# Performance work log

Hardware: AMD Instinct MI355X
Metric: run time of the kernel (lower is better)

The kernel has to match this reference:

```python
import jax, jax.numpy as jnp
import numpy as np

D_MODEL = 512
D_FF = 2048
NUM_EXPERTS = 8
TOP_K = 2


def setup_inputs() -> dict:
    key = jax.random.key(0)
    ks = jax.random.split(key, 6)
    scale = 0.02
    x = jax.random.normal(ks[0], (4, 8192, D_MODEL), dtype=jnp.float32)
    gate_w = jax.random.normal(ks[1], (D_MODEL, NUM_EXPERTS), dtype=jnp.float32) * scale
    w1 = jax.random.normal(ks[2], (NUM_EXPERTS, D_MODEL, D_FF), dtype=jnp.float32) * scale
    b1 = jnp.zeros((NUM_EXPERTS, D_FF), dtype=jnp.float32)
    w2 = jax.random.normal(ks[3], (NUM_EXPERTS, D_FF, D_MODEL), dtype=jnp.float32) * scale
    b2 = jnp.zeros((NUM_EXPERTS, D_MODEL), dtype=jnp.float32)
    return {"x": x, "gate_w": gate_w, "w1": w1, "b1": b1, "w2": w2, "b2": b2}


def reference(x, gate_w, w1, b1, w2, b2):
    B, S, D = x.shape
    xt = x.reshape(-1, D)                                  # [T, D]
    logits = xt @ gate_w                                   # [T, E]
    probs = jax.nn.softmax(logits, axis=-1)
    top_p, top_i = jax.lax.top_k(probs, TOP_K)             # [T, K]
    top_p = top_p / jnp.sum(top_p, axis=-1, keepdims=True)
    # per-token combine weight for each expert: [T, E]
    w_te = jnp.sum(jax.nn.one_hot(top_i, NUM_EXPERTS, dtype=xt.dtype) * top_p[..., None], axis=1)
    out = jnp.zeros_like(xt)
    for e in range(NUM_EXPERTS):  # small fixed loop over experts
        h = jax.nn.gelu(xt @ w1[e] + b1[e], approximate=False)  # [T, d_ff]
        y = h @ w2[e] + b2[e]                                   # [T, D]
        out = out + w_te[:, e:e + 1] * y
    return out.reshape(B, S, D)
```

## Files before the change

kernel.cpp:

```cpp
#include <hip/hip_runtime.h>
#include <math.h>

#define T_TOK 32768
#define DM 512
#define DFF 2048
#define NE 8
#define MAXTILES 528

typedef __attribute__((ext_vector_type(8))) short short8;
typedef __attribute__((ext_vector_type(4))) float f32x4;

__device__ __forceinline__ unsigned int f2bf1(float f) {
  union { float f; unsigned int u; } x; x.f = f;
  return (x.u + 0x7fffu + ((x.u >> 16) & 1u)) >> 16;
}

#define GLOAD(src, dst) \
  __builtin_amdgcn_global_load_lds((const __attribute__((address_space(1))) unsigned int*)(src), \
                                   (__attribute__((address_space(3))) unsigned int*)(dst), 16, 0, 0)
#define WAITVM(N) asm volatile("s_waitcnt vmcnt(" #N ")" ::: "memory")
#define BARRIER() asm volatile("s_barrier" ::: "memory")

__global__ void tcvt_kernel(const float* __restrict__ src, unsigned short* __restrict__ dst,
                            int R, int C) {
  __shared__ float tile[32][33];
  int e = blockIdx.z;
  const float* s = src + (size_t)e * R * C;
  unsigned short* d = dst + (size_t)e * R * C;
  int c0 = blockIdx.x * 32, r0 = blockIdx.y * 32;
  int tx = threadIdx.x, ty = threadIdx.y;
#pragma unroll
  for (int i = 0; i < 4; ++i)
    tile[ty + i * 8][tx] = s[(size_t)(r0 + ty + i * 8) * C + c0 + tx];
  __syncthreads();
#pragma unroll
  for (int i = 0; i < 4; ++i)
    d[(size_t)(c0 + ty + i * 8) * R + r0 + tx] = (unsigned short)f2bf1(tile[tx][ty + i * 8]);
}

__global__ __launch_bounds__(1024) void gate_kernel(
    const float* __restrict__ x, const float* __restrict__ gw,
    int* __restrict__ cnt, int* __restrict__ tok, float* __restrict__ wgt,
    unsigned int* __restrict__ xb) {
  __shared__ int lcnt[NE];
  __shared__ int lbase[NE];
  __shared__ int wslot[16][2];
  __shared__ int winfo[16][2];
  __shared__ float wval[16][2];
  int tid = threadIdx.x;
  int wid = tid >> 6, lane = tid & 63;
  int t = blockIdx.x * 16 + wid;
  if (tid < NE) lcnt[tid] = 0;
  __syncthreads();

  float acc[NE];
#pragma unroll
  for (int e = 0; e < NE; ++e) acc[e] = 0.f;
  const float* xr = x + (size_t)t * DM;
  unsigned int* xbr = xb + (size_t)t * (DM / 2);
#pragma unroll
  for (int j = 0; j < 4; ++j) {
    int d0 = j * 128 + lane * 2;
    float2 xv = *(const float2*)(xr + d0);
    const float* g0 = gw + d0 * NE;
#pragma unroll
    for (int e = 0; e < NE; ++e) acc[e] += xv.x * g0[e] + xv.y * g0[NE + e];
    xbr[j * 64 + lane] = f2bf1(xv.x) | (f2bf1(xv.y) << 16);
  }
#pragma unroll
  for (int off = 32; off >= 1; off >>= 1) {
#pragma unroll
    for (int e = 0; e < NE; ++e) acc[e] += __shfl_xor(acc[e], off);
  }
  if (lane == 0) {
    int e0 = 0; float l0 = acc[0];
#pragma unroll
    for (int e = 1; e < NE; ++e) if (acc[e] > l0) { l0 = acc[e]; e0 = e; }
    int e1 = (e0 == 0) ? 1 : 0; float l1 = acc[e1];
#pragma unroll
    for (int e = 0; e < NE; ++e) if (e != e0 && acc[e] > l1) { l1 = acc[e]; e1 = e; }
    float w0 = 1.f / (1.f + expf(l1 - l0));
    winfo[wid][0] = e0; winfo[wid][1] = e1;
    wval[wid][0] = w0;  wval[wid][1] = 1.f - w0;
    wslot[wid][0] = atomicAdd(&lcnt[e0], 1);
    wslot[wid][1] = atomicAdd(&lcnt[e1], 1);
  }
  __syncthreads();
  if (tid < NE) lbase[tid] = atomicAdd(&cnt[tid * 64], lcnt[tid]);
  __syncthreads();
  if (lane == 0) {
    int e0 = winfo[wid][0], e1 = winfo[wid][1];
    int p0 = lbase[e0] + wslot[wid][0];
    int p1 = lbase[e1] + wslot[wid][1];
    tok[e0 * T_TOK + p0] = t; wgt[e0 * T_TOK + p0] = wval[wid][0];
    tok[e1 * T_TOK + p1] = t; wgt[e1 * T_TOK + p1] = wval[wid][1];
  }
}

__global__ void plan_kernel(const int* __restrict__ cnt, int* __restrict__ tile_base) {
  if (threadIdx.x == 0 && blockIdx.x == 0) {
    int tb = 0;
    for (int e = 0; e < NE; ++e) { tile_base[e] = tb; tb += (cnt[e * 64] + 127) >> 7; }
    tile_base[NE] = tb;
  }
}

__global__ __launch_bounds__(256) void gemm1_kernel(
    const unsigned int* __restrict__ xb, const unsigned short* __restrict__ w1t,
    const float* __restrict__ b1, const int* __restrict__ cnt,
    const int* __restrict__ tok, const int* __restrict__ tile_base,
    unsigned short* __restrict__ H, int tile_lo) {
  int bid = (int)blockIdx.x;
  int nt = bid & 15;
  int gt = tile_lo + (bid >> 4);
  if (gt >= tile_base[NE]) return;
  int e = 0;
#pragma unroll
  for (int k = 0; k < NE - 1; ++k) e += (gt >= tile_base[k + 1]) ? 1 : 0;
  int tloc = gt - tile_base[e];
  int ce = cnt[e * 64];
  int m0 = tloc * 128;
  int n0 = nt * 128;

  __shared__ char Lds[5 * 16384];

  int tid = (int)threadIdx.x;
  int lane = tid & 63;
  int wid = tid >> 6;
  int wm = wid & 1, wn = wid >> 1;
  int fl = lane & 15, q = lane >> 4;
  int sxy = ((q ^ ((fl >> 1) & 3)) << 4);

  const int* tokg = tok + e * T_TOK;
  int r0 = tid >> 2, r1 = 64 + (tid >> 2);
  int sl = tid & 3;
  int ss0 = sl ^ ((r0 >> 1) & 3);
  int ss1 = sl ^ ((r1 >> 1) & 3);
  int t0 = tokg[min(m0 + r0, ce - 1)];
  int t1 = tokg[min(m0 + r1, ce - 1)];
  const char* asrc0 = (const char*)xb + (size_t)t0 * 1024 + ss0 * 16;
  const char* asrc1 = (const char*)xb + (size_t)t1 * 1024 + ss1 * 16;
  const char* bsrc0 = (const char*)w1t + ((size_t)e * DFF + n0 + r0) * 1024 + ss0 * 16;
  const char* bsrc1 = (const char*)w1t + ((size_t)e * DFF + n0 + r1) * 1024 + ss1 * 16;

  int aoff[4], boff[4];
#pragma unroll
  for (int i = 0; i < 4; ++i) {
    aoff[i] = (wm * 64 + i * 16 + fl) * 64 + sxy;
    boff[i] = 8192 + (wn * 64 + i * 16 + fl) * 64 + sxy;
  }

  f32x4 acc[4][4];
#pragma unroll
  for (int a = 0; a < 4; ++a)
#pragma unroll
    for (int b = 0; b < 4; ++b) acc[a][b] = (f32x4){0.f, 0.f, 0.f, 0.f};

#define STAGE1(bi, ti) do { \
    char* base_ = Lds + (bi) * 16384; size_t ko_ = (size_t)(ti) * 64; \
    GLOAD(asrc0 + ko_, base_ + tid * 16);        \
    GLOAD(asrc1 + ko_, base_ + 4096 + tid * 16); \
    GLOAD(bsrc0 + ko_, base_ + 8192 + tid * 16); \
    GLOAD(bsrc1 + ko_, base_ + 12288 + tid * 16); } while (0)

#define COMP1(bi) do { \
    const char* base_ = Lds + (bi) * 16384; \
    short8 a[4], b[4]; \
    _Pragma("unroll") for (int i = 0; i < 4; ++i) { \
      a[i] = *(const short8*)(base_ + aoff[i]); \
      b[i] = *(const short8*)(base_ + boff[i]); } \
    _Pragma("unroll") for (int mf = 0; mf < 4; ++mf) \
    _Pragma("unroll") for (int nf = 0; nf < 4; ++nf) \
      acc[mf][nf] = __builtin_amdgcn_mfma_f32_16x16x32_bf16(a[mf], b[nf], acc[mf][nf], 0, 0, 0); \
  } while (0)

  STAGE1(0, 0); STAGE1(1, 1); STAGE1(2, 2); STAGE1(3, 3);
  int c0 = 0, c1 = 4;
  for (int t = 0; t < 13; ++t) {
    WAITVM(12);
    BARRIER();
    if (t + 4 < 16) { STAGE1(c1, t + 4); c1 = (c1 == 4) ? 0 : c1 + 1; }
    COMP1(c0); c0 = (c0 == 4) ? 0 : c0 + 1;
  }
  WAITVM(8);  BARRIER(); COMP1(c0); c0 = (c0 == 4) ? 0 : c0 + 1;
  WAITVM(4);  BARRIER(); COMP1(c0); c0 = (c0 == 4) ? 0 : c0 + 1;
  WAITVM(0);  BARRIER(); COMP1(c0);
#undef STAGE1
#undef COMP1

  size_t hrow0 = (size_t)(gt - tile_lo) * 128;
#pragma unroll
  for (int nf = 0; nf < 4; ++nf) {
    float bias = b1[e * DFF + n0 + wn * 64 + nf * 16 + fl];
    int col = n0 + wn * 64 + nf * 16 + fl;
#pragma unroll
    for (int mf = 0; mf < 4; ++mf)
#pragma unroll
      for (int j = 0; j < 4; ++j) {
        int row = wm * 64 + mf * 16 + q * 4 + j;
        float v = acc[mf][nf][j] + bias;
        v = 0.5f * v * (1.f + erff(v * 0.70710678118654752f));
        H[(hrow0 + row) * DFF + col] = (unsigned short)f2bf1(v);
      }
  }
}

__global__ __launch_bounds__(256) void gemm2_kernel(
    const unsigned short* __restrict__ H, const unsigned short* __restrict__ w2t,
    const float* __restrict__ b2, const int* __restrict__ cnt,
    const int* __restrict__ tok, const float* __restrict__ wgt,
    const int* __restrict__ tile_base, float* __restrict__ out, int tile_lo) {
  int bid = (int)blockIdx.x;
  int nt = bid & 3;
  int gt = tile_lo + (bid >> 2);
  if (gt >= tile_base[NE]) return;
  int e = 0;
#pragma unroll
  for (int k = 0; k < NE - 1; ++k) e += (gt >= tile_base[k + 1]) ? 1 : 0;
  int tloc = gt - tile_base[e];
  int ce = cnt[e * 64];
  int m0 = tloc * 128;
  int n0 = nt * 128;

  __shared__ char Lds[5 * 16384];

  int tid = (int)threadIdx.x;
  int lane = tid & 63;
  int wid = tid >> 6;
  int wm = wid & 1, wn = wid >> 1;
  int fl = lane & 15, q = lane >> 4;
  int sxy = ((q ^ ((fl >> 1) & 3)) << 4);

  int r0 = tid >> 2, r1 = 64 + (tid >> 2);
  int sl = tid & 3;
  int ss0 = sl ^ ((r0 >> 1) & 3);
  int ss1 = sl ^ ((r1 >> 1) & 3);
  size_t hrow0 = (size_t)(gt - tile_lo) * 128;
  const char* asrc0 = (const char*)H + (hrow0 + r0) * 4096 + ss0 * 16;
  const char* asrc1 = (const char*)H + (hrow0 + r1) * 4096 + ss1 * 16;
  const char* bsrc0 = (const char*)w2t + ((size_t)e * DM + n0 + r0) * 4096 + ss0 * 16;
  const char* bsrc1 = (const char*)w2t + ((size_t)e * DM + n0 + r1) * 4096 + ss1 * 16;

  int aoff[4], boff[4];
#pragma unroll
  for (int i = 0; i < 4; ++i) {
    aoff[i] = (wm * 64 + i * 16 + fl) * 64 + sxy;
    boff[i] = 8192 + (wn * 64 + i * 16 + fl) * 64 + sxy;
  }

  f32x4 acc[4][4];
#pragma unroll
  for (int a = 0; a < 4; ++a)
#pragma unroll
    for (int b = 0; b < 4; ++b) acc[a][b] = (f32x4){0.f, 0.f, 0.f, 0.f};

#define STAGE2(bi, ti) do { \
    char* base_ = Lds + (bi) * 16384; size_t ko_ = (size_t)(ti) * 64; \
    GLOAD(asrc0 + ko_, base_ + tid * 16);        \
    GLOAD(asrc1 + ko_, base_ + 4096 + tid * 16); \
    GLOAD(bsrc0 + ko_, base_ + 8192 + tid * 16); \
    GLOAD(bsrc1 + ko_, base_ + 12288 + tid * 16); } while (0)

#define COMP2(bi) do { \
    const char* base_ = Lds + (bi) * 16384; \
    short8 a[4], b[4]; \
    _Pragma("unroll") for (int i = 0; i < 4; ++i) { \
      a[i] = *(const short8*)(base_ + aoff[i]); \
      b[i] = *(const short8*)(base_ + boff[i]); } \
    _Pragma("unroll") for (int mf = 0; mf < 4; ++mf) \
    _Pragma("unroll") for (int nf = 0; nf < 4; ++nf) \
      acc[mf][nf] = __builtin_amdgcn_mfma_f32_16x16x32_bf16(a[mf], b[nf], acc[mf][nf], 0, 0, 0); \
  } while (0)

  STAGE2(0, 0); STAGE2(1, 1); STAGE2(2, 2); STAGE2(3, 3);
  int c0 = 0, c1 = 4;
  for (int t = 0; t < 61; ++t) {
    WAITVM(12);
    BARRIER();
    if (t + 4 < 64) { STAGE2(c1, t + 4); c1 = (c1 == 4) ? 0 : c1 + 1; }
    COMP2(c0); c0 = (c0 == 4) ? 0 : c0 + 1;
  }
  WAITVM(8);  BARRIER(); COMP2(c0); c0 = (c0 == 4) ? 0 : c0 + 1;
  WAITVM(4);  BARRIER(); COMP2(c0); c0 = (c0 == 4) ? 0 : c0 + 1;
  WAITVM(0);  BARRIER(); COMP2(c0);
#undef STAGE2
#undef COMP2

  const int* tokg = tok + e * T_TOK;
  const float* wgtg = wgt + e * T_TOK;
  float bias2[4];
#pragma unroll
  for (int nf = 0; nf < 4; ++nf) bias2[nf] = b2[e * DM + n0 + wn * 64 + nf * 16 + fl];
#pragma unroll
  for (int mf = 0; mf < 4; ++mf)
#pragma unroll
    for (int j = 0; j < 4; ++j) {
      int row = wm * 64 + mf * 16 + q * 4 + j;
      int slot = m0 + row;
      if (slot < ce) {
        int tk = tokg[slot];
        float w = wgtg[slot];
        float* orow = out + (size_t)tk * DM + n0 + wn * 64;
#pragma unroll
        for (int nf = 0; nf < 4; ++nf)
          atomicAdd(orow + nf * 16 + fl, w * (acc[mf][nf][j] + bias2[nf]));
      }
    }
}

extern "C" void kernel_launch(void* const* d_in, const int* in_sizes, int n_in,
                              void* d_out, int out_size, void* d_ws, size_t ws_size,
                              hipStream_t stream) {
  (void)in_sizes; (void)n_in; (void)out_size;
  const float* x  = (const float*)d_in[0];
  const float* gw = (const float*)d_in[1];
  const float* w1 = (const float*)d_in[2];
  const float* b1 = (const float*)d_in[3];
  const float* w2 = (const float*)d_in[4];
  const float* b2 = (const float*)d_in[5];
  float* out = (float*)d_out;

  char* ws = (char*)d_ws;
  size_t off = 0;
  auto alloc = [&](size_t sz) { char* p = ws + off; off += (sz + 255) & ~(size_t)255; return p; };
  int*   cnt = (int*)alloc(NE * 64 * 4);
  int*   tok = (int*)alloc((size_t)NE * T_TOK * 4);
  float* wgt = (float*)alloc((size_t)NE * T_TOK * 4);
  int*   tile_base = (int*)alloc((NE + 1) * 4);
  unsigned int* xb = (unsigned int*)alloc((size_t)T_TOK * (DM / 2) * 4);
  unsigned short* w1t = (unsigned short*)alloc((size_t)NE * DFF * DM * 2);
  unsigned short* w2t = (unsigned short*)alloc((size_t)NE * DM * DFF * 2);

  size_t avail = (ws_size > off) ? (ws_size - off) : 0;
  int TPC = MAXTILES, NC = 1;
  while (NC < 32 && (size_t)TPC * 128 * DFF * 2 > avail) {
    NC *= 2; TPC = (MAXTILES + NC - 1) / NC;
  }
  unsigned short* H = (unsigned short*)alloc((size_t)TPC * 128 * DFF * 2);

  hipMemsetAsync(cnt, 0, NE * 64 * 4, stream);
  hipMemsetAsync(out, 0, (size_t)T_TOK * DM * 4, stream);

  tcvt_kernel<<<dim3(DFF / 32, DM / 32, NE), dim3(32, 8), 0, stream>>>(w1, w1t, DM, DFF);
  tcvt_kernel<<<dim3(DM / 32, DFF / 32, NE), dim3(32, 8), 0, stream>>>(w2, w2t, DFF, DM);
  gate_kernel<<<T_TOK / 16, 1024, 0, stream>>>(x, gw, cnt, tok, wgt, xb);
  plan_kernel<<<1, 64, 0, stream>>>(cnt, tile_base);

  for (int c = 0; c < NC; ++c) {
    int lo = c * TPC;
    if (lo >= MAXTILES) break;
    gemm1_kernel<<<TPC * 16, 256, 0, stream>>>(xb, w1t, b1, cnt, tok, tile_base, H, lo);
    gemm2_kernel<<<TPC * 4, 256, 0, stream>>>(H, w2t, b2, cnt, tok, wgt, tile_base, out, lo);
  }
}
```

Baseline: 628.4 us.

## Swizzle blocks across XCDs, shrink LDS pipelines, use fast sigmoid-form GELU

Remaps workgroup ids so consecutive tiles spread across the 8 XCDs, improving L2 locality of shared weights and tokens. Reduces LDS staging buffers (3 for gemm1, 4 for gemm2) with unrolled, statically indexed pipelines to raise occupancy and cut index overhead. Replaces exact erf GELU with a tanh-style sigmoid approximation using fast exp, trading accuracy for cheaper epilogue math. Rounds the chunk tile count to even so the swizzle divides evenly.

```diff
diff --git a/kernel.cpp b/kernel.cpp
--- a/kernel.cpp
+++ b/kernel.cpp
@@ -110,7 +110,9 @@
     const float* __restrict__ b1, const int* __restrict__ cnt,
     const int* __restrict__ tok, const int* __restrict__ tile_base,
     unsigned short* __restrict__ H, int tile_lo) {
-  int bid = (int)blockIdx.x;
+  int nwg = (int)gridDim.x;
+  int bid0 = (int)blockIdx.x;
+  int bid = (bid0 & 7) * (nwg >> 3) + (bid0 >> 3);
   int nt = bid & 15;
   int gt = tile_lo + (bid >> 4);
   if (gt >= tile_base[NE]) return;
@@ -122,7 +124,7 @@
   int m0 = tloc * 128;
   int n0 = nt * 128;
 
-  __shared__ char Lds[5 * 16384];
+  __shared__ char Lds[3 * 16384];
 
   int tid = (int)threadIdx.x;
   int lane = tid & 63;
@@ -174,17 +176,16 @@
       acc[mf][nf] = __builtin_amdgcn_mfma_f32_16x16x32_bf16(a[mf], b[nf], acc[mf][nf], 0, 0, 0); \
   } while (0)
 
-  STAGE1(0, 0); STAGE1(1, 1); STAGE1(2, 2); STAGE1(3, 3);
-  int c0 = 0, c1 = 4;
-  for (int t = 0; t < 13; ++t) {
-    WAITVM(12);
+  STAGE1(0, 0); STAGE1(1, 1);
+#pragma unroll
+  for (int t = 0; t < 14; ++t) {
+    WAITVM(4);
     BARRIER();
-    if (t + 4 < 16) { STAGE1(c1, t + 4); c1 = (c1 == 4) ? 0 : c1 + 1; }
-    COMP1(c0); c0 = (c0 == 4) ? 0 : c0 + 1;
-  }
-  WAITVM(8);  BARRIER(); COMP1(c0); c0 = (c0 == 4) ? 0 : c0 + 1;
-  WAITVM(4);  BARRIER(); COMP1(c0); c0 = (c0 == 4) ? 0 : c0 + 1;
-  WAITVM(0);  BARRIER(); COMP1(c0);
+    STAGE1((t + 2) % 3, t + 2);
+    COMP1(t % 3);
+  }
+  WAITVM(4); BARRIER(); COMP1(14 % 3);
+  WAITVM(0); BARRIER(); COMP1(15 % 3);
 #undef STAGE1
 #undef COMP1
 
@@ -199,8 +200,9 @@
       for (int j = 0; j < 4; ++j) {
         int row = wm * 64 + mf * 16 + q * 4 + j;
         float v = acc[mf][nf][j] + bias;
-        v = 0.5f * v * (1.f + erff(v * 0.70710678118654752f));
-        H[(hrow0 + row) * DFF + col] = (unsigned short)f2bf1(v);
+        float u2 = v * (1.5957691216f + 0.0713548162f * v * v);
+        float g = v / (1.f + __expf(-u2));
+        H[(hrow0 + row) * DFF + col] = (unsigned short)f2bf1(g);
       }
   }
 }
@@ -210,7 +212,9 @@
     const float* __restrict__ b2, const int* __restrict__ cnt,
     const int* __restrict__ tok, const float* __restrict__ wgt,
     const int* __restrict__ tile_base, float* __restrict__ out, int tile_lo) {
-  int bid = (int)blockIdx.x;
+  int nwg = (int)gridDim.x;
+  int bid0 = (int)blockIdx.x;
+  int bid = (bid0 & 7) * (nwg >> 3) + (bid0 >> 3);
   int nt = bid & 3;
   int gt = tile_lo + (bid >> 2);
   if (gt >= tile_base[NE]) return;
@@ -222,7 +226,7 @@
   int m0 = tloc * 128;
   int n0 = nt * 128;
 
-  __shared__ char Lds[5 * 16384];
+  __shared__ char Lds[4 * 16384];
 
   int tid = (int)threadIdx.x;
   int lane = tid & 63;
@@ -272,17 +276,21 @@
       acc[mf][nf] = __builtin_amdgcn_mfma_f32_16x16x32_bf16(a[mf], b[nf], acc[mf][nf], 0, 0, 0); \
   } while (0)
 
-  STAGE2(0, 0); STAGE2(1, 1); STAGE2(2, 2); STAGE2(3, 3);
-  int c0 = 0, c1 = 4;
-  for (int t = 0; t < 61; ++t) {
-    WAITVM(12);
-    BARRIER();
-    if (t + 4 < 64) { STAGE2(c1, t + 4); c1 = (c1 == 4) ? 0 : c1 + 1; }
-    COMP2(c0); c0 = (c0 == 4) ? 0 : c0 + 1;
-  }
-  WAITVM(8);  BARRIER(); COMP2(c0); c0 = (c0 == 4) ? 0 : c0 + 1;
-  WAITVM(4);  BARRIER(); COMP2(c0); c0 = (c0 == 4) ? 0 : c0 + 1;
-  WAITVM(0);  BARRIER(); COMP2(c0);
+#define STEP2(t, sb, cb) do { \
+    WAITVM(8); BARRIER(); STAGE2(sb, (t) + 3); COMP2(cb); } while (0)
+
+  STAGE2(0, 0); STAGE2(1, 1); STAGE2(2, 2);
+  for (int tt = 0; tt < 60; tt += 4) {
+    STEP2(tt + 0, 3, 0);
+    STEP2(tt + 1, 0, 1);
+    STEP2(tt + 2, 1, 2);
+    STEP2(tt + 3, 2, 3);
+  }
+  WAITVM(8); BARRIER(); STAGE2(3, 63); COMP2(0);
+  WAITVM(8); BARRIER(); COMP2(1);
+  WAITVM(4); BARRIER(); COMP2(2);
+  WAITVM(0); BARRIER(); COMP2(3);
+#undef STEP2
 #undef STAGE2
 #undef COMP2
 
@@ -334,7 +342,8 @@
   size_t avail = (ws_size > off) ? (ws_size - off) : 0;
   int TPC = MAXTILES, NC = 1;
   while (NC < 32 && (size_t)TPC * 128 * DFF * 2 > avail) {
-    NC *= 2; TPC = (MAXTILES + NC - 1) / NC;
+    NC *= 2;
+    TPC = (((MAXTILES + NC - 1) / NC) + 1) & ~1;
   }
   unsigned short* H = (unsigned short*)alloc((size_t)TPC * 128 * DFF * 2);
 
@@ -346,9 +355,8 @@
   gate_kernel<<<T_TOK / 16, 1024, 0, stream>>>(x, gw, cnt, tok, wgt, xb);
   plan_kernel<<<1, 64, 0, stream>>>(cnt, tile_base);
 
-  for (int c = 0; c < NC; ++c) {
+  for (int c = 0; c * TPC < MAXTILES; ++c) {
     int lo = c * TPC;
-    if (lo >= MAXTILES) break;
     gemm1_kernel<<<TPC * 16, 256, 0, stream>>>(xb, w1t, b1, cnt, tok, tile_base, H, lo);
     gemm2_kernel<<<TPC * 4, 256, 0, stream>>>(H, w2t, b2, cnt, tok, wgt, tile_base, out, lo);
   }
```

Result: faster. 600.8 us (-4.4%).
